# Kernel optimization log

Measured on AMD Instinct MI355X. Metric: run time of the kernel, lower is better.

The kernel has to match this reference:

```python
import jax, jax.numpy as jnp
import numpy as np

N_EMBD = 768
HEAD_SIZE = 72
SEQ_LEN = 512
BATCH = 64

def setup_inputs() -> dict:
    key = jax.random.key(0)
    kx, kk, kq, kv = jax.random.split(key, 4)
    # Linear weights stored as [in, out] for x @ W; torch Linear init ~ U(-1/sqrt(in), 1/sqrt(in))
    bound = 1.0 / np.sqrt(N_EMBD)
    x = jax.random.normal(kx, (BATCH, SEQ_LEN, N_EMBD), dtype=jnp.float32)
    Wk = jax.random.uniform(kk, (N_EMBD, HEAD_SIZE), minval=-bound, maxval=bound, dtype=jnp.float32)
    Wq = jax.random.uniform(kq, (N_EMBD, HEAD_SIZE), minval=-bound, maxval=bound, dtype=jnp.float32)
    Wv = jax.random.uniform(kv, (N_EMBD, HEAD_SIZE), minval=-bound, maxval=bound, dtype=jnp.float32)
    return {"x": x, "Wk": Wk, "Wq": Wq, "Wv": Wv}

def reference(x, Wk, Wq, Wv):
    # Single causal self-attention head (dropout in eval mode = identity).
    k = x @ Wk  # [B, T, H]
    q = x @ Wq  # [B, T, H]
    v = x @ Wv  # [B, T, H]
    scale = k.shape[-1] ** (-0.5)
    scores = jnp.einsum('bth,bsh->bts', q, k) * scale  # [B, T, T]
    T = scores.shape[-1]
    causal = jnp.tril(jnp.ones((T, T), dtype=bool))
    scores = jnp.where(causal, scores, -jnp.inf)
    attn = jax.nn.softmax(scores, axis=-1)
    out = jnp.einsum('bts,bsh->bth', attn, v)  # [B, T, H]
    return out
```

## Files before the change

kernel.cpp:

```cpp
#include <hip/hip_runtime.h>


typedef short bf16x8 __attribute__((ext_vector_type(8)));
typedef float f32x4 __attribute__((ext_vector_type(4)));
typedef float f32x4v __attribute__((ext_vector_type(4)));

#define DEVI __device__ __forceinline__
#define SB0() __builtin_amdgcn_sched_barrier(0)

DEVI unsigned f2bf(float f) {
  unsigned u = __builtin_bit_cast(unsigned, f);
  return (u + 0x7fffu + ((u >> 16) & 1u)) >> 16;
}
DEVI unsigned pk2(float a, float b) { return f2bf(a) | (f2bf(b) << 16); }

DEVI void async16(void* lds, const void* g) {
  __builtin_amdgcn_global_load_lds(
      (const __attribute__((address_space(1))) unsigned int*)g,
      (__attribute__((address_space(3))) unsigned int*)lds, 16, 0, 0);
}

__global__ __launch_bounds__(256) void cast_w_k(const float* __restrict__ Wk,
                                                const float* __restrict__ Wq,
                                                const float* __restrict__ Wv,
                                                unsigned short* __restrict__ wbt) {
  __shared__ float ldsT[72][65];
  const int mat = blockIdx.x / 12, kc = blockIdx.x % 12;
  const float* W = (mat == 0) ? Wk : (mat == 1) ? Wq : Wv;
  const float sc = (mat == 1) ? 0.11785113019775793f : 1.0f;
  const float* src = W + kc * 64 * 72;
  for (int i = threadIdx.x; i < 1152; i += 256) {
    float4 d = *(const float4*)(src + i * 4);
    int e = i * 4;
    ldsT[e % 72][e / 72] = d.x;
    ldsT[(e + 1) % 72][(e + 1) / 72] = d.y;
    ldsT[(e + 2) % 72][(e + 2) / 72] = d.z;
    ldsT[(e + 3) % 72][(e + 3) / 72] = d.w;
  }
  __syncthreads();
  for (int c = threadIdx.x; c < 640; c += 256) {
    int h = c >> 3, kb = (c & 7) * 8;
    uint4 o = {0u, 0u, 0u, 0u};
    if (h < 72) {
      const float* rowp = &ldsT[h][kb];
      o.x = pk2(rowp[0] * sc, rowp[1] * sc);
      o.y = pk2(rowp[2] * sc, rowp[3] * sc);
      o.z = pk2(rowp[4] * sc, rowp[5] * sc);
      o.w = pk2(rowp[6] * sc, rowp[7] * sc);
    }
    *(uint4*)(wbt + ((size_t)mat * 80 + h) * 768 + kc * 64 + kb) = o;
  }
}

struct ProjSmem {
  union {
    struct {
      short x[2][64 * 64];
      short w[2][240 * 64];
    } s;
    short t[80 * 72];
  };
};

__global__ __launch_bounds__(256, 2) void proj_k(
    const float* __restrict__ x, const unsigned short* __restrict__ wbt,
    unsigned short* __restrict__ Kg, unsigned short* __restrict__ Qg,
    unsigned short* __restrict__ Vt) {
  __shared__ __align__(16) ProjSmem sm;
  const int row0 = blockIdx.x * 64;
  const int tid = threadIdx.x, wave = tid >> 6, lane = tid & 63;
  const int quad = lane >> 4, l16 = lane & 15;
  const int mg = wave >> 1, ng = wave & 1;
  const int ntile0 = ng * 8, ntn = ng ? 7 : 8;

  const int t0row = tid >> 3, tcb = tid & 7;
  const int wr8 = lane >> 3, wcb = lane & 7;

  f32x4 acc[2][8] = {};

  f32x4v xa0[2], xb0[2], xa1[2], xb1[2];

  auto issue_x = [&](int k0, f32x4v* Ar, f32x4v* Br) {
    const float* g0 = x + (size_t)(row0 + t0row) * 768 + k0 + tcb * 8;
    Ar[0] = *(const f32x4v*)g0;
    Br[0] = *(const f32x4v*)(g0 + 4);
    const float* g1 = g0 + (size_t)32 * 768;
    Ar[1] = *(const f32x4v*)g1;
    Br[1] = *(const f32x4v*)(g1 + 4);
  };
  auto issue_w = [&](int k0, int nb) {
#pragma unroll
    for (int j = 0; j < 8; ++j) {
      int inst = j * 4 + wave;
      if (inst < 30) {
        int r = inst * 8 + wr8;
        async16(&sm.s.w[nb][inst * 512],
                wbt + (size_t)r * 768 + k0 + ((wcb ^ (r & 7)) * 8));
      }
    }
  };
  auto write_x = [&](int nb, const f32x4v* Ar, const f32x4v* Br) {
    uint4 o0 = {pk2(Ar[0].x, Ar[0].y), pk2(Ar[0].z, Ar[0].w),
                pk2(Br[0].x, Br[0].y), pk2(Br[0].z, Br[0].w)};
    *(uint4*)&sm.s.x[nb][t0row * 64 + ((tcb ^ (t0row & 7)) * 8)] = o0;
    int r1 = t0row + 32;
    uint4 o1 = {pk2(Ar[1].x, Ar[1].y), pk2(Ar[1].z, Ar[1].w),
                pk2(Br[1].x, Br[1].y), pk2(Br[1].z, Br[1].w)};
    *(uint4*)&sm.s.x[nb][r1 * 64 + ((tcb ^ (r1 & 7)) * 8)] = o1;
  };
  auto compute = [&](int cb) {
#pragma unroll
    for (int ks = 0; ks < 2; ++ks) {
      const int pblk = ((ks << 2) | quad) ^ (l16 & 7);
      bf16x8 af[2];
#pragma unroll
      for (int mt = 0; mt < 2; ++mt)
        af[mt] = *(const bf16x8*)&sm.s.x[cb][(mg * 32 + mt * 16 + l16) * 64 + pblk * 8];
#pragma unroll
      for (int j = 0; j < 8; ++j)
        if (j < ntn) {
          int nt = ntile0 + j;
          bf16x8 bfr = *(const bf16x8*)&sm.s.w[cb][(nt * 16 + l16) * 64 + pblk * 8];
          acc[0][j] = __builtin_amdgcn_mfma_f32_16x16x32_bf16(af[0], bfr, acc[0][j], 0, 0, 0);
          acc[1][j] = __builtin_amdgcn_mfma_f32_16x16x32_bf16(af[1], bfr, acc[1][j], 0, 0, 0);
        }
    }
  };

  issue_w(0, 0);
  SB0();
  issue_x(0, xa0, xb0);
  write_x(0, xa0, xb0);
  SB0();
  issue_x(64, xa1, xb1);
  SB0();
  asm volatile("s_waitcnt vmcnt(4) lgkmcnt(0)" ::: "memory");
  SB0();
  __builtin_amdgcn_s_barrier();

  for (int t = 0; t < 10; t += 2) {
    issue_w((t + 1) * 64, 1);
    SB0();
    issue_x((t + 2) * 64, xa0, xb0);
    SB0();
    compute(0);
    write_x(1, xa1, xb1);
    asm volatile("s_waitcnt vmcnt(4) lgkmcnt(0)" ::: "memory");
    SB0();
    __builtin_amdgcn_s_barrier();
    issue_w((t + 2) * 64, 0);
    SB0();
    issue_x((t + 3) * 64, xa1, xb1);
    SB0();
    compute(1);
    write_x(0, xa0, xb0);
    asm volatile("s_waitcnt vmcnt(4) lgkmcnt(0)" ::: "memory");
    SB0();
    __builtin_amdgcn_s_barrier();
  }
  issue_w(11 * 64, 1);
  SB0();
  compute(0);
  write_x(1, xa1, xb1);
  asm volatile("s_waitcnt vmcnt(0) lgkmcnt(0)" ::: "memory");
  SB0();
  __builtin_amdgcn_s_barrier();
  compute(1);
  __syncthreads();

#pragma unroll
  for (int mt = 0; mt < 2; ++mt)
#pragma unroll
    for (int r = 0; r < 4; ++r) {
      int lrow64 = mg * 32 + mt * 16 + quad * 4 + r;
      size_t grow = (size_t)row0 + lrow64;
#pragma unroll
      for (int j = 0; j < 8; ++j)
        if (j < ntn) {
          int nt = ntile0 + j;
          float v = acc[mt][j][r];
          if (nt < 5) {
            Kg[grow * 104 + nt * 16 + l16] = (unsigned short)f2bf(v);
          } else if (nt < 10) {
            Qg[grow * 104 + (nt - 5) * 16 + l16] = (unsigned short)f2bf(v);
          } else {
            sm.t[((nt - 10) * 16 + l16) * 72 + lrow64] = (short)f2bf(v);
          }
        }
      unsigned short* p = (ng ? Qg : Kg) + grow * 104;
      p[80 + l16] = 0;
      if (l16 < 8) p[96 + l16] = 0;
    }
  __syncthreads();
  int b = blockIdx.x >> 3, t0 = (blockIdx.x & 7) * 64;
  const uint4 ones = {0x3F803F80u, 0x3F803F80u, 0x3F803F80u, 0x3F803F80u};
  for (int c = tid; c < 640; c += 256) {
    int hr = c >> 3, tc = (c & 7) * 8;
    uint4 d = *(const uint4*)&sm.t[hr * 72 + tc];
    if (hr == 72) d = ones;
    *(uint4*)(Vt + ((size_t)b * 80 + hr) * 512 + t0 + tc) = d;
  }
}

__global__ __launch_bounds__(256, 2) void attn_k(
    const unsigned short* __restrict__ Qg, const unsigned short* __restrict__ Kg,
    const unsigned short* __restrict__ Vt, float* __restrict__ out) {
  __shared__ __align__(16) short lk[2][64 * 104];
  __shared__ __align__(16) short lv[2][80 * 64];
  __shared__ __align__(16) short lp[4][16 * 72];

  int idx = (blockIdx.x < 256) ? blockIdx.x : 767 - blockIdx.x;
  const int qb = 7 - (idx >> 6), b = idx & 63;
  const int tid = threadIdx.x, wave = tid >> 6, lane = tid & 63;
  const int quad = lane >> 4, l16 = lane & 15;
  const int lrow = lane >> 3, lcb = lane & 7;
  const int trow0 = qb * 64 + wave * 16;

  bf16x8 qf[3];
#pragma unroll
  for (int kt = 0; kt < 3; ++kt)
    qf[kt] = *(const bf16x8*)(Qg + ((size_t)b * 512 + trow0 + l16) * 104 + kt * 32 + quad * 8);

  auto stage = [&](int kb, int pb) {
    const int s0 = kb * 64;
#pragma unroll
    for (int j = 0; j < 4; ++j) {
      int inst = j * 4 + wave;
      if (inst < 13)
        async16(&lk[pb][inst * 512], Kg + ((size_t)b * 512 + s0) * 104 + inst * 512 + lane * 8);
    }
    for (int j = wave; j < 10; j += 4) {
      int r = j * 8 + lrow;
      async16(&lv[pb][j * 512], Vt + ((size_t)b * 80 + r) * 512 + s0 + (lcb ^ lrow) * 8);
    }
  };

  f32x4 o[5] = {};

  stage(0, 0);
  asm volatile("s_waitcnt vmcnt(0)" ::: "memory");
  SB0();
  __builtin_amdgcn_s_barrier();

  for (int kb = 0; kb <= qb; ++kb) {
    const int pb = kb & 1;
    const int s0 = kb * 64;
    const bool diag = (kb == qb);
    const int nact = diag ? (wave + 1) : 4;

    if (!diag) stage(kb + 1, pb ^ 1);
    SB0();

    f32x4 sacc[4] = {};
#pragma unroll
    for (int kt = 0; kt < 3; ++kt)
      for (int nt = 0; nt < nact; ++nt) {
        bf16x8 kf = *(const bf16x8*)&lk[pb][(nt * 16 + l16) * 104 + kt * 32 + quad * 8];
        sacc[nt] = __builtin_amdgcn_mfma_f32_16x16x32_bf16(qf[kt], kf, sacc[nt], 0, 0, 0);
      }
    if (diag) {
      int nt = wave;
#pragma unroll
      for (int r = 0; r < 4; ++r) {
        int t = trow0 + quad * 4 + r;
        if (s0 + nt * 16 + l16 > t) sacc[nt][r] = -1e30f;
      }
    }
#pragma unroll
    for (int nt = 0; nt < 4; ++nt)
#pragma unroll
      for (int r = 0; r < 4; ++r) {
        float p = (nt < nact) ? __expf(sacc[nt][r]) : 0.0f;
        lp[wave][(quad * 4 + r) * 72 + nt * 16 + l16] = (short)f2bf(p);
      }
#pragma unroll
    for (int ks = 0; ks < 2; ++ks) {
      bf16x8 pf = *(const bf16x8*)&lp[wave][l16 * 72 + ks * 32 + quad * 8];
      const int pblk = ((ks << 2) | quad) ^ (l16 & 7);
#pragma unroll
      for (int nt = 0; nt < 5; ++nt) {
        bf16x8 vf = *(const bf16x8*)&lv[pb][(nt * 16 + l16) * 64 + pblk * 8];
        o[nt] = __builtin_amdgcn_mfma_f32_16x16x32_bf16(pf, vf, o[nt], 0, 0, 0);
      }
    }
    if (!diag) {
      asm volatile("s_waitcnt vmcnt(0) lgkmcnt(0)" ::: "memory");
      SB0();
      __builtin_amdgcn_s_barrier();
    }
  }

#pragma unroll
  for (int r = 0; r < 4; ++r) {
    float l = __shfl(o[4][r], (lane & 48) | 8, 64);
    float inv = 1.0f / l;
    size_t t = (size_t)b * 512 + trow0 + quad * 4 + r;
#pragma unroll
    for (int nt = 0; nt < 5; ++nt) {
      int h = nt * 16 + l16;
      if (h < 72) out[t * 72 + h] = o[nt][r] * inv;
    }
  }
}

extern "C" void kernel_launch(void* const* d_in, const int* in_sizes, int n_in,
                              void* d_out, int out_size, void* d_ws, size_t ws_size,
                              hipStream_t stream) {
  const float* x  = (const float*)d_in[0];
  const float* Wk = (const float*)d_in[1];
  const float* Wq = (const float*)d_in[2];
  const float* Wv = (const float*)d_in[3];
  float* out = (float*)d_out;

  char* ws = (char*)d_ws;
  unsigned short* Kg  = (unsigned short*)(ws);
  unsigned short* Qg  = (unsigned short*)(ws + 6815744);
  unsigned short* Vt  = (unsigned short*)(ws + 13631488);
  unsigned short* wbt = (unsigned short*)(ws + 18874368);

  cast_w_k<<<36, 256, 0, stream>>>(Wk, Wq, Wv, wbt);
  proj_k<<<512, 256, 0, stream>>>(x, wbt, Kg, Qg, Vt);
  attn_k<<<512, 256, 0, stream>>>(Qg, Kg, Vt, out);
}
```

Baseline: 189.3 us.

## Load K and V fragments directly from global memory instead of LDS staging

Result: slower. 203.0 us (+7.3%).

```diff
diff --git a/kernel.cpp b/kernel.cpp
--- a/kernel.cpp
+++ b/kernel.cpp
@@ -205,15 +205,12 @@
 __global__ __launch_bounds__(256, 2) void attn_k(
     const unsigned short* __restrict__ Qg, const unsigned short* __restrict__ Kg,
     const unsigned short* __restrict__ Vt, float* __restrict__ out) {
-  __shared__ __align__(16) short lk[2][64 * 104];
-  __shared__ __align__(16) short lv[2][80 * 64];
   __shared__ __align__(16) short lp[4][16 * 72];
 
   int idx = (blockIdx.x < 256) ? blockIdx.x : 767 - blockIdx.x;
   const int qb = 7 - (idx >> 6), b = idx & 63;
   const int tid = threadIdx.x, wave = tid >> 6, lane = tid & 63;
   const int quad = lane >> 4, l16 = lane & 15;
-  const int lrow = lane >> 3, lcb = lane & 7;
   const int trow0 = qb * 64 + wave * 16;
 
   bf16x8 qf[3];
@@ -221,41 +218,21 @@
   for (int kt = 0; kt < 3; ++kt)
     qf[kt] = *(const bf16x8*)(Qg + ((size_t)b * 512 + trow0 + l16) * 104 + kt * 32 + quad * 8);
 
-  auto stage = [&](int kb, int pb) {
-    const int s0 = kb * 64;
-#pragma unroll
-    for (int j = 0; j < 4; ++j) {
-      int inst = j * 4 + wave;
-      if (inst < 13)
-        async16(&lk[pb][inst * 512], Kg + ((size_t)b * 512 + s0) * 104 + inst * 512 + lane * 8);
-    }
-    for (int j = wave; j < 10; j += 4) {
-      int r = j * 8 + lrow;
-      async16(&lv[pb][j * 512], Vt + ((size_t)b * 80 + r) * 512 + s0 + (lcb ^ lrow) * 8);
-    }
-  };
+  const unsigned short* Krow = Kg + ((size_t)b * 512 + l16) * 104;
+  const unsigned short* Vrow = Vt + ((size_t)b * 80 + l16) * 512;
 
   f32x4 o[5] = {};
 
-  stage(0, 0);
-  asm volatile("s_waitcnt vmcnt(0)" ::: "memory");
-  SB0();
-  __builtin_amdgcn_s_barrier();
-
   for (int kb = 0; kb <= qb; ++kb) {
-    const int pb = kb & 1;
     const int s0 = kb * 64;
     const bool diag = (kb == qb);
     const int nact = diag ? (wave + 1) : 4;
 
-    if (!diag) stage(kb + 1, pb ^ 1);
-    SB0();
-
     f32x4 sacc[4] = {};
 #pragma unroll
     for (int kt = 0; kt < 3; ++kt)
       for (int nt = 0; nt < nact; ++nt) {
-        bf16x8 kf = *(const bf16x8*)&lk[pb][(nt * 16 + l16) * 104 + kt * 32 + quad * 8];
+        bf16x8 kf = *(const bf16x8*)(Krow + (size_t)(s0 + nt * 16) * 104 + kt * 32 + quad * 8);
         sacc[nt] = __builtin_amdgcn_mfma_f32_16x16x32_bf16(qf[kt], kf, sacc[nt], 0, 0, 0);
       }
     if (diag) {
@@ -276,17 +253,11 @@
 #pragma unroll
     for (int ks = 0; ks < 2; ++ks) {
       bf16x8 pf = *(const bf16x8*)&lp[wave][l16 * 72 + ks * 32 + quad * 8];
-      const int pblk = ((ks << 2) | quad) ^ (l16 & 7);
 #pragma unroll
       for (int nt = 0; nt < 5; ++nt) {
-        bf16x8 vf = *(const bf16x8*)&lv[pb][(nt * 16 + l16) * 64 + pblk * 8];
+        bf16x8 vf = *(const bf16x8*)(Vrow + (size_t)(nt * 16) * 512 + s0 + (((ks << 2) | quad)) * 8);
         o[nt] = __builtin_amdgcn_mfma_f32_16x16x32_bf16(pf, vf, o[nt], 0, 0, 0);
       }
-    }
-    if (!diag) {
-      asm volatile("s_waitcnt vmcnt(0) lgkmcnt(0)" ::: "memory");
-      SB0();
-      __builtin_amdgcn_s_barrier();
     }
   }
 
```
